# Kernel tuning notes

Measured on AMD Instinct MI355X. Metric: run time of the kernel, lower is better.

Reference implementation:

```python
import jax, jax.numpy as jnp
import numpy as np

S1 = (42, 1600, 1408); S2 = (21, 800, 704); S3 = (11, 400, 352); S4 = (6, 200, 176)
OFF = np.array([[dz, dy, dx] for dz in (-1, 0, 1) for dy in (-1, 0, 1) for dx in (-1, 0, 1)], np.int64)
KOFF = np.array([[kz, ky, kx] for kz in (0, 1, 2) for ky in (0, 1, 2) for kx in (0, 1, 2)], np.int64)

def _keys(c, s):
    return (c[:, 0] * s[1] + c[:, 1]) * s[2] + c[:, 2]

def _lookup(skeys, qk, valid):
    pos = np.searchsorted(skeys, qk)
    posc = np.clip(pos, 0, len(skeys) - 1)
    found = valid & (skeys[posc] == qk)
    return np.where(found, posc, -1).astype(np.int32)

def _subm_nbr(coords, skeys, shape):
    N = len(coords); nbr = np.empty((N, 27), np.int32); sh = np.array(shape)
    for t in range(27):
        q = coords + OFF[t]
        valid = np.all((q >= 0) & (q < sh), axis=1)
        nbr[:, t] = _lookup(skeys, _keys(q, shape), valid)
    return nbr

def _inv_nbr(fcoords, ckeys, cshape):
    # inverse of stride-2, pad-1, k-3 sparse conv: coarse = (fine + 1 - k) / 2
    N = len(fcoords); nbr = np.empty((N, 27), np.int32); csh = np.array(cshape)
    for t in range(27):
        cand = fcoords + 1 - KOFF[t]
        valid = np.all(cand >= 0, axis=1) & np.all(cand % 2 == 0, axis=1)
        cc = cand // 2
        valid &= np.all(cc < csh, axis=1)
        nbr[:, t] = _lookup(ckeys, _keys(cc, cshape), valid)
    return nbr

def _geometry():
    rng = np.random.default_rng(0)
    n = 130000
    c = np.stack([rng.integers(0, S1[i], n) for i in range(3)], 1).astype(np.int64)
    uk, idx = np.unique(_keys(c, S1), return_index=True)
    c1 = c[idx][:100000]; k1 = uk[:len(c1)]
    def down(cf, s):
        cc = cf // 2
        uk, idx = np.unique(_keys(cc, s), return_index=True)
        return cc[idx], uk
    c2, k2 = down(c1, S2); c3, k3 = down(c2, S3); c4, k4 = down(c3, S4)
    return dict(nbr4=_subm_nbr(c4, k4, S4), inv43=_inv_nbr(c3, k4, S4),
                nbr3=_subm_nbr(c3, k3, S3), inv32=_inv_nbr(c2, k3, S3),
                nbr2=_subm_nbr(c2, k2, S2), inv21=_inv_nbr(c1, k2, S2),
                nbr1=_subm_nbr(c1, k1, S1), n4=len(c4), n1=len(c1))

_SPECS = [("m4", 64, 64), ("i4", 64, 64), ("m3", 64, 64), ("i3", 64, 32),
          ("m2", 32, 32), ("i2", 32, 16), ("m1", 16, 16), ("c5", 16, 3)]

def _params(key):
    p = {}
    for i, (nm, ci, co) in enumerate(_SPECS):
        k = jax.random.fold_in(key, i)
        p["W_" + nm] = jax.random.normal(k, (27, ci, co), jnp.float32) * (1.0 / np.sqrt(27.0 * ci))
        p["g_" + nm] = jnp.ones((co,), jnp.float32)
        p["b_" + nm] = jnp.zeros((co,), jnp.float32)
    return p

def setup_inputs() -> dict:
    geo = _geometry()
    key = jax.random.key(0)
    inp = {k: jnp.asarray(v) for k, v in geo.items() if k.startswith(("nbr", "inv"))}
    inp["x"] = jax.random.normal(jax.random.fold_in(key, 100), (geo["n4"], 64), jnp.float32)
    inp.update(_params(key))
    return inp

def _block(f, nbr, W, g, b, relu=True):
    # gather-GEMM (sparse conv), then BatchNorm1d (training mode, eps=1e-3), then ReLU
    m = nbr >= 0                                             # [N,27]
    x = jnp.where(m[..., None], f[jnp.maximum(nbr, 0)], 0.0)  # [N,27,Cin]
    y = jnp.einsum('nkc,kcd->nd', x, W)                      # [N,Cout]
    mu = y.mean(0); var = y.var(0)
    y = (y - mu) * jax.lax.rsqrt(var + 1e-3) * g + b
    return jax.nn.relu(y) if relu else y

def reference(x, nbr4, inv43, nbr3, inv32, nbr2, inv21, nbr1,
              W_m4, g_m4, b_m4, W_i4, g_i4, b_i4, W_m3, g_m3, b_m3, W_i3, g_i3, b_i3,
              W_m2, g_m2, b_m2, W_i2, g_i2, b_i2, W_m1, g_m1, b_m1, W_c5, g_c5, b_c5):
    h = _block(x, nbr4, W_m4, g_m4, b_m4)      # subm4: [N4,64]
    h = _block(h, inv43, W_i4, g_i4, b_i4)     # inverse conv4 -> [N3,64]
    h = _block(h, nbr3, W_m3, g_m3, b_m3)      # subm3
    h = _block(h, inv32, W_i3, g_i3, b_i3)     # inverse conv3 -> [N2,32]
    h = _block(h, nbr2, W_m2, g_m2, b_m2)      # subm2
    h = _block(h, inv21, W_i2, g_i2, b_i2)     # inverse conv2 -> [N1,16]
    h = _block(h, nbr1, W_m1, g_m1, b_m1)      # subm1
    return _block(h, nbr1, W_c5, g_c5, b_c5, relu=False)  # conv5 (shares subm1 rulebook), BN only
```

## Files before the change

### kernel.cpp

```cpp
#include <hip/hip_runtime.h>

typedef _Float16 HALF;
typedef _Float16 f16x8 __attribute__((ext_vector_type(8)));
typedef float f32x4 __attribute__((ext_vector_type(4)));
typedef int i32x4 __attribute__((ext_vector_type(4)));

struct WArgs { const float* W[8]; HALF* dst[8]; };

__global__ void convert_all_w_kernel(WArgs a)
{
    const int CIs[8]  = {64, 64, 64, 64, 32, 32, 16, 16};
    const int COs[8]  = {64, 64, 64, 32, 32, 16, 16, 3};
    const int COPs[8] = {64, 64, 64, 32, 32, 16, 16, 16};
    const int L = blockIdx.y;
    const int CI = CIs[L], CO = COs[L], COP = COPs[L];
    const int K = 27 * CI, KP = (K + 31) & ~31;
    const int total = COP * KP;
    for (int i = blockIdx.x * 256 + threadIdx.x; i < total; i += gridDim.x * 256) {
        int jp = i / KP;
        int kp = i - jp * KP;
        float v = (jp < CO && kp < K) ? a.W[L][(size_t)kp * CO + jp] : 0.f;
        a.dst[L][((size_t)(kp >> 5) * COP + jp) * 32 + (kp & 31)] = (HALF)v;
    }
}

__global__ void convert_x_kernel(const float* __restrict__ x, HALF* __restrict__ xh, int total)
{
    int i = blockIdx.x * 256 + threadIdx.x;
    if (i < total) xh[i] = (HALF)x[i];
}

template<int CI, int CO_PAD, int NMT, bool FUSED>
__global__ __launch_bounds__(256, 2) void conv_kernel(
    const HALF* __restrict__ h, const int* __restrict__ nbr,
    const HALF* __restrict__ Wt, HALF* __restrict__ yout,
    float* __restrict__ sums, int n,
    const float* __restrict__ psums, const float* __restrict__ pg,
    const float* __restrict__ pb, float pinvn)
{
    constexpr int K    = 27 * CI;
    constexpr int KP   = (K + 31) & ~31;
    constexpr int NCH  = KP / 32;
    constexpr int NJB  = CO_PAD / 16;
    constexpr int NW   = 4;
    constexpr int CHK  = (NCH + NW - 1) / NW;
    constexpr int NCB  = (CI >= 64) ? 2 : 1;
    static_assert(NCB == 1 || (CHK & 1) == 0, "parity must stay compile-time");
    constexpr int LOG2CI = (CI == 64) ? 6 : ((CI == 32) ? 5 : 4);
    constexpr int ROWS  = 16 * NMT;
    constexpr int PAIRS = NMT * NJB;
    constexpr int TPW   = CHK / 2;

    __shared__ f32x4 lred[2][PAIRS * 64];
    __shared__ float lscbi[2][64];

    const int wv   = threadIdx.x >> 6;
    const int lane = threadIdx.x & 63;
    const int l15  = lane & 15;
    const int lq   = lane >> 4;

    int bid = blockIdx.x;
    {
        const int nwg = gridDim.x;
        const int q = nwg >> 3, r = nwg & 7;
        const int xcd = bid & 7, idx = bid >> 3;
        bid = (xcd < r ? xcd * (q + 1) : r * (q + 1) + (xcd - r) * q) + idx;
    }
    const int rowBase = bid * ROWS;

    if constexpr (FUSED) {
        const int c = threadIdx.x;
        if (c < CI) {
            float s = 0.f, q = 0.f;
#pragma unroll
            for (int k = 0; k < 8; ++k) { s += psums[k * 128 + c]; q += psums[k * 128 + CI + c]; }
            const float mu  = s * pinvn;
            const float var = q * pinvn - mu * mu;
            const float sc  = rsqrtf(var + 1e-3f) * pg[c];
            lscbi[0][c] = sc;
            lscbi[1][c] = pb[c] - mu * sc;
        }
    }

    f32x4 acc[NMT][NJB];
#pragma unroll
    for (int mt = 0; mt < NMT; ++mt)
#pragma unroll
        for (int jb = 0; jb < NJB; ++jb)
#pragma unroll
            for (int r = 0; r < 4; ++r) acc[mt][jb][r] = 0.f;

    int  nbo[NMT];
    bool rok[NMT];
#pragma unroll
    for (int mt = 0; mt < NMT; ++mt) {
        const int row = rowBase + mt * 16 + l15;
        rok[mt] = row < n;
        nbo[mt] = min(row, n - 1) * 27;
    }

    if constexpr (FUSED) __syncthreads();

    f16x8 sc8[NCB], bi8[NCB];
    if constexpr (FUSED) {
#pragma unroll
        for (int cb = 0; cb < NCB; ++cb) {
            const int c0 = cb * 32 + ((lq * 8) & (CI - 1));
#pragma unroll
            for (int j = 0; j < 8; ++j) {
                sc8[cb][j] = (HALF)lscbi[0][c0 + j];
                bi8[cb][j] = (HALF)lscbi[1][c0 + j];
            }
        }
    }

    if constexpr (CI == 64) {
        const int t0 = wv * TPW;

        int   ipf[2][NMT];
        f16x8 apf[2][NMT][2];
#pragma unroll
        for (int p = 0; p < 2; ++p) {
            const int t = t0 + p;
#pragma unroll
            for (int mt = 0; mt < NMT; ++mt) {
                const int v   = nbr[nbo[mt] + (t < 27 ? t : 26)];
                const int idx = (rok[mt] && t < 27) ? v : -1;
                ipf[p][mt] = idx;
                const HALF* pa = h + ((max(idx, 0) << 6) + lq * 8);
                apf[p][mt][0] = *(const f16x8*)(pa);
                apf[p][mt][1] = *(const f16x8*)(pa + 32);
            }
        }

#pragma unroll
        for (int tt = 0; tt < TPW; ++tt) {
            const int t = t0 + tt;
            if (t >= 27) break;
            const int cur = tt & 1;

            f16x8 a0[NMT], a1[NMT]; int im[NMT];
#pragma unroll
            for (int mt = 0; mt < NMT; ++mt) {
                a0[mt] = apf[cur][mt][0]; a1[mt] = apf[cur][mt][1]; im[mt] = ipf[cur][mt];
            }

            if (tt + 2 < TPW && t + 2 < 27) {
#pragma unroll
                for (int mt = 0; mt < NMT; ++mt) {
                    const int v   = nbr[nbo[mt] + t + 2];
                    const int idx = rok[mt] ? v : -1;
                    ipf[cur][mt] = idx;
                    const HALF* pa = h + ((max(idx, 0) << 6) + lq * 8);
                    apf[cur][mt][0] = *(const f16x8*)(pa);
                    apf[cur][mt][1] = *(const f16x8*)(pa + 32);
                }
            }

            const HALF* wb = Wt + (size_t)(2 * t) * (CO_PAD * 32) + lq * 8;
            f16x8 b0[NJB], b1[NJB];
#pragma unroll
            for (int jb = 0; jb < NJB; ++jb) {
                b0[jb] = *(const f16x8*)(wb + (size_t)(jb * 16 + l15) * 32);
                b1[jb] = *(const f16x8*)(wb + CO_PAD * 32 + (size_t)(jb * 16 + l15) * 32);
            }

#pragma unroll
            for (int mt = 0; mt < NMT; ++mt) {
                f16x8 a = a0[mt];
                if constexpr (FUSED) {
                    a = a * sc8[0] + bi8[0];
#pragma unroll
                    for (int j = 0; j < 8; ++j) a[j] = (a[j] < (HALF)0.f) ? (HALF)0.f : a[j];
                }
                const int m = ~(im[mt] >> 31);
                i32x4 ai = __builtin_bit_cast(i32x4, a);
                ai.x &= m; ai.y &= m; ai.z &= m; ai.w &= m;
                a = __builtin_bit_cast(f16x8, ai);
#pragma unroll
                for (int jb = 0; jb < NJB; ++jb)
                    acc[mt][jb] = __builtin_amdgcn_mfma_f32_16x16x32_f16(a, b0[jb], acc[mt][jb], 0, 0, 0);
            }
#pragma unroll
            for (int mt = 0; mt < NMT; ++mt) {
                f16x8 a = a1[mt];
                if constexpr (FUSED) {
                    a = a * sc8[NCB - 1] + bi8[NCB - 1];
#pragma unroll
                    for (int j = 0; j < 8; ++j) a[j] = (a[j] < (HALF)0.f) ? (HALF)0.f : a[j];
                }
                const int m = ~(im[mt] >> 31);
                i32x4 ai = __builtin_bit_cast(i32x4, a);
                ai.x &= m; ai.y &= m; ai.z &= m; ai.w &= m;
                a = __builtin_bit_cast(f16x8, ai);
#pragma unroll
                for (int jb = 0; jb < NJB; ++jb)
                    acc[mt][jb] = __builtin_amdgcn_mfma_f32_16x16x32_f16(a, b1[jb], acc[mt][jb], 0, 0, 0);
            }
        }
    } else {
        const int kc0 = wv * CHK;

        int   ipf[2][NMT];
        f16x8 apf[2][NMT];
#pragma unroll
        for (int p = 0; p < 2; ++p) {
            const int kc = kc0 + p;
#pragma unroll
            for (int mt = 0; mt < NMT; ++mt) {
                const int t   = (CI == 16) ? (2 * kc + (lq >> 1)) : kc;
                const int v   = nbr[nbo[mt] + (t < 27 ? t : 26)];
                const int idx = (rok[mt] && t < 27) ? v : -1;
                ipf[p][mt] = idx;
                const int c = (CI == 32) ? (lq * 8) : ((lq & 1) * 8);
                apf[p][mt] = *(const f16x8*)(h + ((max(idx, 0) << LOG2CI) + c));
            }
        }

#pragma unroll
        for (int kc2 = 0; kc2 < CHK; ++kc2) {
            const int kc = kc0 + kc2;
            if (kc >= NCH) break;
            const int cur = kc2 & 1;

            const HALF* wb = Wt + (size_t)kc * (CO_PAD * 32) + lq * 8;
            f16x8 b[NJB];
#pragma unroll
            for (int jb = 0; jb < NJB; ++jb)
                b[jb] = *(const f16x8*)(wb + (size_t)(jb * 16 + l15) * 32);

            f16x8 a_use[NMT];
            int   i_use[NMT];
#pragma unroll
            for (int mt = 0; mt < NMT; ++mt) { a_use[mt] = apf[cur][mt]; i_use[mt] = ipf[cur][mt]; }

            if (kc2 + 2 < CHK && kc + 2 < NCH) {
#pragma unroll
                for (int mt = 0; mt < NMT; ++mt) {
                    const int t   = (CI == 16) ? (2 * (kc + 2) + (lq >> 1)) : (kc + 2);
                    const int v   = nbr[nbo[mt] + (t < 27 ? t : 26)];
                    const int idx = (rok[mt] && t < 27) ? v : -1;
                    ipf[cur][mt] = idx;
                    const int c = (CI == 32) ? (lq * 8) : ((lq & 1) * 8);
                    apf[cur][mt] = *(const f16x8*)(h + ((max(idx, 0) << LOG2CI) + c));
                }
            }

#pragma unroll
            for (int mt = 0; mt < NMT; ++mt) {
                f16x8 a = a_use[mt];
                if constexpr (FUSED) {
                    a = a * sc8[0] + bi8[0];
#pragma unroll
                    for (int j = 0; j < 8; ++j) a[j] = (a[j] < (HALF)0.f) ? (HALF)0.f : a[j];
                }
                const int m = ~(i_use[mt] >> 31);
                i32x4 ai = __builtin_bit_cast(i32x4, a);
                ai.x &= m; ai.y &= m; ai.z &= m; ai.w &= m;
                a = __builtin_bit_cast(f16x8, ai);
#pragma unroll
                for (int jb = 0; jb < NJB; ++jb)
                    acc[mt][jb] = __builtin_amdgcn_mfma_f32_16x16x32_f16(a, b[jb], acc[mt][jb], 0, 0, 0);
            }
        }
    }

    if (wv & 1) {
#pragma unroll
        for (int mt = 0; mt < NMT; ++mt)
#pragma unroll
            for (int jb = 0; jb < NJB; ++jb)
                lred[wv >> 1][(mt * NJB + jb) * 64 + lane] = acc[mt][jb];
    }
    __syncthreads();
    if (!(wv & 1)) {
#pragma unroll
        for (int mt = 0; mt < NMT; ++mt)
#pragma unroll
            for (int jb = 0; jb < NJB; ++jb)
                acc[mt][jb] += lred[wv >> 1][(mt * NJB + jb) * 64 + lane];
    }
    __syncthreads();
    if (wv == 2) {
#pragma unroll
        for (int mt = 0; mt < NMT; ++mt)
#pragma unroll
            for (int jb = 0; jb < NJB; ++jb)
                lred[0][(mt * NJB + jb) * 64 + lane] = acc[mt][jb];
    }
    __syncthreads();

    if (wv == 0) {
#pragma unroll
        for (int mt = 0; mt < NMT; ++mt)
#pragma unroll
            for (int jb = 0; jb < NJB; ++jb)
                acc[mt][jb] += lred[0][(mt * NJB + jb) * 64 + lane];

        float* sl = sums + (bid & 7) * 128;
#pragma unroll
        for (int jb = 0; jb < NJB; ++jb) {
            const int col = jb * 16 + l15;
            float s = 0.f, sq = 0.f;
#pragma unroll
            for (int mt = 0; mt < NMT; ++mt) {
                const int rb = rowBase + mt * 16 + lq * 4;
#pragma unroll
                for (int r = 0; r < 4; ++r) {
                    if (rb + r < n) {
                        const float v = acc[mt][jb][r];
                        yout[(size_t)(rb + r) * CO_PAD + col] = (HALF)v;
                        s += v;
                        sq += v * v;
                    }
                }
            }
            s  += __shfl_xor(s, 16);  s  += __shfl_xor(s, 32);
            sq += __shfl_xor(sq, 16); sq += __shfl_xor(sq, 32);
            if (lane < 16) {
                atomicAdd(&sl[col], s);
                atomicAdd(&sl[CO_PAD + col], sq);
            }
        }
    }
}

__global__ void bn_out_kernel(const HALF* __restrict__ y, const float* __restrict__ sums,
                              const float* __restrict__ g, const float* __restrict__ b,
                              int n, float invn, float* __restrict__ out)
{
    int i = blockIdx.x * 256 + threadIdx.x;
    if (i >= n * 3) return;
    int row = i / 3;
    int c = i - row * 3;
    float ssum = 0.f, qsum = 0.f;
#pragma unroll
    for (int k2 = 0; k2 < 8; ++k2) {
        ssum += sums[k2 * 128 + c];
        qsum += sums[k2 * 128 + 16 + c];
    }
    float mu  = ssum * invn;
    float var = qsum * invn - mu * mu;
    float sc  = rsqrtf(var + 1e-3f) * g[c];
    out[i] = ((float)y[(size_t)row * 16 + c] - mu) * sc + b[c];
}

extern "C" void kernel_launch(void* const* d_in, const int* in_sizes, int n_in,
                              void* d_out, int out_size, void* d_ws, size_t ws_size,
                              hipStream_t stream)
{
    const int* nbr4  = (const int*)d_in[0];
    const int* inv43 = (const int*)d_in[1];
    const int* nbr3  = (const int*)d_in[2];
    const int* inv32 = (const int*)d_in[3];
    const int* nbr2  = (const int*)d_in[4];
    const int* inv21 = (const int*)d_in[5];
    const int* nbr1  = (const int*)d_in[6];
    const float* x   = (const float*)d_in[7];

    const int n4 = in_sizes[0] / 27;
    const int n3 = in_sizes[1] / 27;
    const int n2 = in_sizes[3] / 27;
    const int n1 = in_sizes[5] / 27;

    const int CIs[8]  = {64, 64, 64, 64, 32, 32, 16, 16};
    const int COPs[8] = {64, 64, 64, 32, 32, 16, 16, 16};
    int KPs[8], wtoff[8];
    int wtot = 0;
    for (int s = 0; s < 8; ++s) {
        KPs[s] = ((27 * CIs[s] + 31) / 32) * 32;
        wtoff[s] = wtot;
        wtot += COPs[s] * KPs[s];
    }

    char* ws = (char*)d_ws;
    HALF* wt = (HALF*)ws;
    size_t off = ((size_t)wtot * sizeof(HALF) + 255) & ~(size_t)255;
    float* sums = (float*)(ws + off);
    off += 8 * 1024 * sizeof(float);
    off = (off + 255) & ~(size_t)255;
    HALF* xh = (HALF*)(ws + off);
    off += ((size_t)n4 * 64 * sizeof(HALF) + 255) & ~(size_t)255;
    size_t bufElems = 0;
    {
        size_t cand[4] = {(size_t)n4 * 64, (size_t)n3 * 64, (size_t)n2 * 32, (size_t)n1 * 16};
        for (int i = 0; i < 4; ++i) if (cand[i] > bufElems) bufElems = cand[i];
    }
    HALF* Y0 = (HALF*)(ws + off);
    off += (bufElems * sizeof(HALF) + 255) & ~(size_t)255;
    HALF* Y1 = (HALF*)(ws + off);

    hipMemsetAsync(sums, 0, 8 * 1024 * sizeof(float), stream);

    WArgs wa;
    for (int s = 0; s < 8; ++s) { wa.W[s] = (const float*)d_in[8 + 3 * s]; wa.dst[s] = wt + wtoff[s]; }
    {
        int maxTotal = 64 * KPs[0];
        dim3 grid((maxTotal + 255) / 256, 8);
        convert_all_w_kernel<<<grid, 256, 0, stream>>>(wa);
    }
    convert_x_kernel<<<(n4 * 64 + 255) / 256, 256, 0, stream>>>(x, xh, n4 * 64);

#define G(s) ((const float*)d_in[9 + 3 * (s)])
#define B(s) ((const float*)d_in[10 + 3 * (s)])
#define SUMS(s) (sums + (s) * 1024)
#define GRID(nn) (((nn) + 31) / 32)

    conv_kernel<64, 64, 2, false><<<GRID(n4), 256, 0, stream>>>(
        xh, nbr4, wt + wtoff[0], Y0, SUMS(0), n4, nullptr, nullptr, nullptr, 0.f);
    conv_kernel<64, 64, 2, true><<<GRID(n3), 256, 0, stream>>>(
        Y0, inv43, wt + wtoff[1], Y1, SUMS(1), n3, SUMS(0), G(0), B(0), 1.f / n4);
    conv_kernel<64, 64, 2, true><<<GRID(n3), 256, 0, stream>>>(
        Y1, nbr3, wt + wtoff[2], Y0, SUMS(2), n3, SUMS(1), G(1), B(1), 1.f / n3);
    conv_kernel<64, 32, 2, true><<<GRID(n2), 256, 0, stream>>>(
        Y0, inv32, wt + wtoff[3], Y1, SUMS(3), n2, SUMS(2), G(2), B(2), 1.f / n3);
    conv_kernel<32, 32, 2, true><<<GRID(n2), 256, 0, stream>>>(
        Y1, nbr2, wt + wtoff[4], Y0, SUMS(4), n2, SUMS(3), G(3), B(3), 1.f / n2);
    conv_kernel<32, 16, 2, true><<<GRID(n1), 256, 0, stream>>>(
        Y0, inv21, wt + wtoff[5], Y1, SUMS(5), n1, SUMS(4), G(4), B(4), 1.f / n2);
    conv_kernel<16, 16, 2, true><<<GRID(n1), 256, 0, stream>>>(
        Y1, nbr1, wt + wtoff[6], Y0, SUMS(6), n1, SUMS(5), G(5), B(5), 1.f / n1);
    conv_kernel<16, 16, 2, true><<<GRID(n1), 256, 0, stream>>>(
        Y0, nbr1, wt + wtoff[7], Y1, SUMS(7), n1, SUMS(6), G(6), B(6), 1.f / n1);
    bn_out_kernel<<<(n1 * 3 + 255) / 256, 256, 0, stream>>>(
        Y1, SUMS(7), G(7), B(7), n1, 1.f / n1, (float*)d_out);

#undef G
#undef B
#undef SUMS
#undef GRID
}
```

Before: 482.8 us.

## Stage neighbor indices in LDS and skip taps empty across a row tile

Each 32-row block now loads its neighbor indices into shared memory once. It then builds a compacted list of kernel taps that have at least one valid neighbor in the tile, and waves walk only those taps, so gathers, weight loads and MFMAs for fully empty taps are skipped. The geometry is very sparse (random points, inverse convs), so many taps should be empty. In exchange the kernel adds extra barriers, a serial single-thread compaction step, and a dynamic loop that replaces the fully unrolled static prefetch schedule on the non-full paths.

```diff
diff --git a/kernel.cpp b/kernel.cpp
--- a/kernel.cpp
+++ b/kernel.cpp
@@ -30,7 +30,7 @@
     if (i < total) xh[i] = (HALF)x[i];
 }
 
-template<int CI, int CO_PAD, int NMT, bool FUSED>
+template<int CI, int CO_PAD, bool FUSED>
 __global__ __launch_bounds__(256, 2) void conv_kernel(
     const HALF* __restrict__ h, const int* __restrict__ nbr,
     const HALF* __restrict__ Wt, HALF* __restrict__ yout,
@@ -38,21 +38,19 @@
     const float* __restrict__ psums, const float* __restrict__ pg,
     const float* __restrict__ pb, float pinvn)
 {
-    constexpr int K    = 27 * CI;
-    constexpr int KP   = (K + 31) & ~31;
-    constexpr int NCH  = KP / 32;
-    constexpr int NJB  = CO_PAD / 16;
-    constexpr int NW   = 4;
-    constexpr int CHK  = (NCH + NW - 1) / NW;
-    constexpr int NCB  = (CI >= 64) ? 2 : 1;
-    static_assert(NCB == 1 || (CHK & 1) == 0, "parity must stay compile-time");
+    constexpr int NMT   = 2;
+    constexpr int NJB   = CO_PAD / 16;
+    constexpr int NCB   = (CI >= 64) ? 2 : 1;
     constexpr int LOG2CI = (CI == 64) ? 6 : ((CI == 32) ? 5 : 4);
-    constexpr int ROWS  = 16 * NMT;
+    constexpr int ROWS  = 32;
     constexpr int PAIRS = NMT * NJB;
-    constexpr int TPW   = CHK / 2;
 
     __shared__ f32x4 lred[2][PAIRS * 64];
     __shared__ float lscbi[2][64];
+    __shared__ int   lidx[ROWS * 27];
+    __shared__ int   tflag[27];
+    __shared__ int   tls[32];
+    __shared__ int   ntapS;
 
     const int wv   = threadIdx.x >> 6;
     const int lane = threadIdx.x & 63;
@@ -68,6 +66,11 @@
     }
     const int rowBase = bid * ROWS;
 
+    for (int i = threadIdx.x; i < ROWS * 27; i += 256) {
+        const int r   = i / 27;
+        const int row = rowBase + r;
+        lidx[i] = (row < n) ? nbr[(size_t)row * 27 + (i - r * 27)] : -1;
+    }
     if constexpr (FUSED) {
         const int c = threadIdx.x;
         if (c < CI) {
@@ -81,25 +84,23 @@
             lscbi[1][c] = pb[c] - mu * sc;
         }
     }
-
-    f32x4 acc[NMT][NJB];
-#pragma unroll
-    for (int mt = 0; mt < NMT; ++mt)
-#pragma unroll
-        for (int jb = 0; jb < NJB; ++jb)
-#pragma unroll
-            for (int r = 0; r < 4; ++r) acc[mt][jb][r] = 0.f;
-
-    int  nbo[NMT];
-    bool rok[NMT];
-#pragma unroll
-    for (int mt = 0; mt < NMT; ++mt) {
-        const int row = rowBase + mt * 16 + l15;
-        rok[mt] = row < n;
-        nbo[mt] = min(row, n - 1) * 27;
-    }
-
-    if constexpr (FUSED) __syncthreads();
+    __syncthreads();
+
+    if (threadIdx.x < 27) {
+        int any = 0;
+        for (int r = 0; r < ROWS; ++r) any |= ~(lidx[r * 27 + threadIdx.x] >> 31);
+        tflag[threadIdx.x] = any & 1;
+    }
+    __syncthreads();
+    if (threadIdx.x == 0) {
+        int c = 0;
+#pragma unroll
+        for (int t = 0; t < 27; ++t) if (tflag[t]) tls[c++] = t;
+        ntapS = c;
+        for (int t = c; t < 32; ++t) tls[t] = 27;
+    }
+    __syncthreads();
+    const int NT = ntapS;
 
     f16x8 sc8[NCB], bi8[NCB];
     if constexpr (FUSED) {
@@ -114,156 +115,216 @@
         }
     }
 
+    f32x4 acc[NMT][NJB];
+#pragma unroll
+    for (int mt = 0; mt < NMT; ++mt)
+#pragma unroll
+        for (int jb = 0; jb < NJB; ++jb)
+#pragma unroll
+            for (int r = 0; r < 4; ++r) acc[mt][jb][r] = 0.f;
+
+    int lb[NMT];
+#pragma unroll
+    for (int mt = 0; mt < NMT; ++mt) lb[mt] = (mt * 16 + l15) * 27;
+
+    #define CONSUME64(aV_, imV_, bV_, CBIDX_) do { \
+        f16x8 a_ = (aV_); \
+        if constexpr (FUSED) { \
+            a_ = a_ * sc8[CBIDX_] + bi8[CBIDX_]; \
+            _Pragma("unroll") \
+            for (int j_ = 0; j_ < 8; ++j_) a_[j_] = (a_[j_] < (HALF)0.f) ? (HALF)0.f : a_[j_]; \
+        } \
+        const int m_ = ~((imV_) >> 31); \
+        i32x4 ai_ = __builtin_bit_cast(i32x4, a_); \
+        ai_.x &= m_; ai_.y &= m_; ai_.z &= m_; ai_.w &= m_; \
+        a_ = __builtin_bit_cast(f16x8, ai_); \
+        _Pragma("unroll") \
+        for (int jb_ = 0; jb_ < NJB; ++jb_) \
+            acc[mt][jb_] = __builtin_amdgcn_mfma_f32_16x16x32_f16(a_, (bV_)[jb_], acc[mt][jb_], 0, 0, 0); \
+    } while (0)
+
     if constexpr (CI == 64) {
-        const int t0 = wv * TPW;
-
-        int   ipf[2][NMT];
-        f16x8 apf[2][NMT][2];
-#pragma unroll
-        for (int p = 0; p < 2; ++p) {
-            const int t = t0 + p;
+        if (NT == 27) {
+            constexpr int TPW = 7;
+            const int t0 = wv * TPW;
+
+            int   ipf[2][NMT];
+            f16x8 apf[2][NMT][2];
+#pragma unroll
+            for (int p = 0; p < 2; ++p) {
+                const int t = t0 + p;
+#pragma unroll
+                for (int mt = 0; mt < NMT; ++mt) {
+                    const int idx = (t < 27) ? lidx[lb[mt] + (t < 27 ? t : 26)] : -1;
+                    ipf[p][mt] = idx;
+                    const HALF* pa = h + ((max(idx, 0) << 6) + lq * 8);
+                    apf[p][mt][0] = *(const f16x8*)(pa);
+                    apf[p][mt][1] = *(const f16x8*)(pa + 32);
+                }
+            }
+
+#pragma unroll
+            for (int tt = 0; tt < TPW; ++tt) {
+                const int t = t0 + tt;
+                if (t >= 27) break;
+                const int cur = tt & 1;
+
+                f16x8 a0[NMT], a1[NMT]; int im[NMT];
+#pragma unroll
+                for (int mt = 0; mt < NMT; ++mt) {
+                    a0[mt] = apf[cur][mt][0]; a1[mt] = apf[cur][mt][1]; im[mt] = ipf[cur][mt];
+                }
+
+                if (tt + 2 < TPW && t + 2 < 27) {
+#pragma unroll
+                    for (int mt = 0; mt < NMT; ++mt) {
+                        const int idx = lidx[lb[mt] + t + 2];
+                        ipf[cur][mt] = idx;
+                        const HALF* pa = h + ((max(idx, 0) << 6) + lq * 8);
+                        apf[cur][mt][0] = *(const f16x8*)(pa);
+                        apf[cur][mt][1] = *(const f16x8*)(pa + 32);
+                    }
+                }
+
+                const HALF* wb = Wt + (size_t)(2 * t) * (CO_PAD * 32) + lq * 8;
+                f16x8 b0[NJB], b1[NJB];
+#pragma unroll
+                for (int jb = 0; jb < NJB; ++jb) {
+                    b0[jb] = *(const f16x8*)(wb + (size_t)(jb * 16 + l15) * 32);
+                    b1[jb] = *(const f16x8*)(wb + CO_PAD * 32 + (size_t)(jb * 16 + l15) * 32);
+                }
+
+#pragma unroll
+                for (int mt = 0; mt < NMT; ++mt) CONSUME64(a0[mt], im[mt], b0, 0);
+#pragma unroll
+                for (int mt = 0; mt < NMT; ++mt) CONSUME64(a1[mt], im[mt], b1, NCB - 1);
+            }
+        } else {
+            int ti = wv;
+            int   tcur, icur[NMT];
+            f16x8 a0c[NMT], a1c[NMT];
+            {
+                tcur = tls[ti];
+#pragma unroll
+                for (int mt = 0; mt < NMT; ++mt) {
+                    const int idx = (tcur < 27) ? lidx[lb[mt] + min(tcur, 26)] : -1;
+                    icur[mt] = idx;
+                    const HALF* pa = h + ((max(idx, 0) << 6) + lq * 8);
+                    a0c[mt] = *(const f16x8*)(pa);
+                    a1c[mt] = *(const f16x8*)(pa + 32);
+                }
+            }
+            for (; ti < NT; ti += 4) {
+                int   tnx = tls[min(ti + 4, 31)];
+                int   inx[NMT];
+                f16x8 a0n[NMT], a1n[NMT];
+#pragma unroll
+                for (int mt = 0; mt < NMT; ++mt) {
+                    const int idx = (tnx < 27) ? lidx[lb[mt] + min(tnx, 26)] : -1;
+                    inx[mt] = idx;
+                    const HALF* pa = h + ((max(idx, 0) << 6) + lq * 8);
+                    a0n[mt] = *(const f16x8*)(pa);
+                    a1n[mt] = *(const f16x8*)(pa + 32);
+                }
+
+                const HALF* wb = Wt + (size_t)(2 * tcur) * (CO_PAD * 32) + lq * 8;
+                f16x8 b0[NJB], b1[NJB];
+#pragma unroll
+                for (int jb = 0; jb < NJB; ++jb) {
+                    b0[jb] = *(const f16x8*)(wb + (size_t)(jb * 16 + l15) * 32);
+                    b1[jb] = *(const f16x8*)(wb + CO_PAD * 32 + (size_t)(jb * 16 + l15) * 32);
+                }
+
+#pragma unroll
+                for (int mt = 0; mt < NMT; ++mt) CONSUME64(a0c[mt], icur[mt], b0, 0);
+#pragma unroll
+                for (int mt = 0; mt < NMT; ++mt) CONSUME64(a1c[mt], icur[mt], b1, NCB - 1);
+
+                tcur = tnx;
+#pragma unroll
+                for (int mt = 0; mt < NMT; ++mt) {
+                    icur[mt] = inx[mt]; a0c[mt] = a0n[mt]; a1c[mt] = a1n[mt];
+                }
+            }
+        }
+    } else if constexpr (CI == 32) {
+        int ti = wv;
+        int   tcur, icur[NMT];
+        f16x8 ac[NMT];
+        {
+            tcur = tls[ti];
 #pragma unroll
             for (int mt = 0; mt < NMT; ++mt) {
-                const int v   = nbr[nbo[mt] + (t < 27 ? t : 26)];
-                const int idx = (rok[mt] && t < 27) ? v : -1;
-                ipf[p][mt] = idx;
-                const HALF* pa = h + ((max(idx, 0) << 6) + lq * 8);
-                apf[p][mt][0] = *(const f16x8*)(pa);
-                apf[p][mt][1] = *(const f16x8*)(pa + 32);
-            }
-        }
-
-#pragma unroll
-        for (int tt = 0; tt < TPW; ++tt) {
-            const int t = t0 + tt;
-            if (t >= 27) break;
-            const int cur = tt & 1;
-
-            f16x8 a0[NMT], a1[NMT]; int im[NMT];
+                const int idx = (tcur < 27) ? lidx[lb[mt] + min(tcur, 26)] : -1;
+                icur[mt] = idx;
+                ac[mt] = *(const f16x8*)(h + ((max(idx, 0) << 5) + lq * 8));
+            }
+        }
+        for (; ti < NT; ti += 4) {
+            int   tnx = tls[min(ti + 4, 31)];
+            int   inx[NMT];
+            f16x8 an[NMT];
 #pragma unroll
             for (int mt = 0; mt < NMT; ++mt) {
-                a0[mt] = apf[cur][mt][0]; a1[mt] = apf[cur][mt][1]; im[mt] = ipf[cur][mt];
-            }
-
-            if (tt + 2 < TPW && t + 2 < 27) {
-#pragma unroll
-                for (int mt = 0; mt < NMT; ++mt) {
-                    const int v   = nbr[nbo[mt] + t + 2];
-                    const int idx = rok[mt] ? v : -1;
-                    ipf[cur][mt] = idx;
-                    const HALF* pa = h + ((max(idx, 0) << 6) + lq * 8);
-                    apf[cur][mt][0] = *(const f16x8*)(pa);
-                    apf[cur][mt][1] = *(const f16x8*)(pa + 32);
-                }
-            }
-
-            const HALF* wb = Wt + (size_t)(2 * t) * (CO_PAD * 32) + lq * 8;
-            f16x8 b0[NJB], b1[NJB];
-#pragma unroll
-            for (int jb = 0; jb < NJB; ++jb) {
-                b0[jb] = *(const f16x8*)(wb + (size_t)(jb * 16 + l15) * 32);
-                b1[jb] = *(const f16x8*)(wb + CO_PAD * 32 + (size_t)(jb * 16 + l15) * 32);
-            }
-
+                const int idx = (tnx < 27) ? lidx[lb[mt] + min(tnx, 26)] : -1;
+                inx[mt] = idx;
+                an[mt] = *(const f16x8*)(h + ((max(idx, 0) << 5) + lq * 8));
+            }
+
+            const HALF* wb = Wt + (size_t)tcur * (CO_PAD * 32) + lq * 8;
+            f16x8 b[NJB];
+#pragma unroll
+            for (int jb = 0; jb < NJB; ++jb)
+                b[jb] = *(const f16x8*)(wb + (size_t)(jb * 16 + l15) * 32);
+
+#pragma unroll
+            for (int mt = 0; mt < NMT; ++mt) CONSUME64(ac[mt], icur[mt], b, 0);
+
+            tcur = tnx;
+#pragma unroll
+            for (int mt = 0; mt < NMT; ++mt) { icur[mt] = inx[mt]; ac[mt] = an[mt]; }
+        }
+    } else {
+        const int NS = (NT + 1) >> 1;
+        int ti = wv;
+        int   tcur, icur[NMT];
+        f16x8 ac[NMT];
+        {
+            tcur = tls[min(2 * ti + (lq >> 1), 31)];
 #pragma unroll
             for (int mt = 0; mt < NMT; ++mt) {
-                f16x8 a = a0[mt];
-                if constexpr (FUSED) {
-                    a = a * sc8[0] + bi8[0];
-#pragma unroll
-                    for (int j = 0; j < 8; ++j) a[j] = (a[j] < (HALF)0.f) ? (HALF)0.f : a[j];
-                }
-                const int m = ~(im[mt] >> 31);
-                i32x4 ai = __builtin_bit_cast(i32x4, a);
-                ai.x &= m; ai.y &= m; ai.z &= m; ai.w &= m;
-                a = __builtin_bit_cast(f16x8, ai);
-#pragma unroll
-                for (int jb = 0; jb < NJB; ++jb)
-                    acc[mt][jb] = __builtin_amdgcn_mfma_f32_16x16x32_f16(a, b0[jb], acc[mt][jb], 0, 0, 0);
-            }
+                const int idx = (tcur < 27) ? lidx[lb[mt] + min(tcur, 26)] : -1;
+                icur[mt] = idx;
+                ac[mt] = *(const f16x8*)(h + ((max(idx, 0) << 4) + (lq & 1) * 8));
+            }
+        }
+        for (; ti < NS; ti += 4) {
+            int   tnx = tls[min(2 * (ti + 4) + (lq >> 1), 31)];
+            int   inx[NMT];
+            f16x8 an[NMT];
 #pragma unroll
             for (int mt = 0; mt < NMT; ++mt) {
-                f16x8 a = a1[mt];
-                if constexpr (FUSED) {
-                    a = a * sc8[NCB - 1] + bi8[NCB - 1];
-#pragma unroll
-                    for (int j = 0; j < 8; ++j) a[j] = (a[j] < (HALF)0.f) ? (HALF)0.f : a[j];
-                }
-                const int m = ~(im[mt] >> 31);
-                i32x4 ai = __builtin_bit_cast(i32x4, a);
-                ai.x &= m; ai.y &= m; ai.z &= m; ai.w &= m;
-                a = __builtin_bit_cast(f16x8, ai);
-#pragma unroll
-                for (int jb = 0; jb < NJB; ++jb)
-                    acc[mt][jb] = __builtin_amdgcn_mfma_f32_16x16x32_f16(a, b1[jb], acc[mt][jb], 0, 0, 0);
-            }
-        }
-    } else {
-        const int kc0 = wv * CHK;
-
-        int   ipf[2][NMT];
-        f16x8 apf[2][NMT];
-#pragma unroll
-        for (int p = 0; p < 2; ++p) {
-            const int kc = kc0 + p;
-#pragma unroll
-            for (int mt = 0; mt < NMT; ++mt) {
-                const int t   = (CI == 16) ? (2 * kc + (lq >> 1)) : kc;
-                const int v   = nbr[nbo[mt] + (t < 27 ? t : 26)];
-                const int idx = (rok[mt] && t < 27) ? v : -1;
-                ipf[p][mt] = idx;
-                const int c = (CI == 32) ? (lq * 8) : ((lq & 1) * 8);
-                apf[p][mt] = *(const f16x8*)(h + ((max(idx, 0) << LOG2CI) + c));
-            }
-        }
-
-#pragma unroll
-        for (int kc2 = 0; kc2 < CHK; ++kc2) {
-            const int kc = kc0 + kc2;
-            if (kc >= NCH) break;
-            const int cur = kc2 & 1;
-
-            const HALF* wb = Wt + (size_t)kc * (CO_PAD * 32) + lq * 8;
+                const int idx = (tnx < 27) ? lidx[lb[mt] + min(tnx, 26)] : -1;
+                inx[mt] = idx;
+                an[mt] = *(const f16x8*)(h + ((max(idx, 0) << 4) + (lq & 1) * 8));
+            }
+
+            const int tb = min(tcur, 26);
             f16x8 b[NJB];
 #pragma unroll
             for (int jb = 0; jb < NJB; ++jb)
-                b[jb] = *(const f16x8*)(wb + (size_t)(jb * 16 + l15) * 32);
-
-            f16x8 a_use[NMT];
-            int   i_use[NMT];
-#pragma unroll
-            for (int mt = 0; mt < NMT; ++mt) { a_use[mt] = apf[cur][mt]; i_use[mt] = ipf[cur][mt]; }
-
-            if (kc2 + 2 < CHK && kc + 2 < NCH) {
-#pragma unroll
-                for (int mt = 0; mt < NMT; ++mt) {
-                    const int t   = (CI == 16) ? (2 * (kc + 2) + (lq >> 1)) : (kc + 2);
-                    const int v   = nbr[nbo[mt] + (t < 27 ? t : 26)];
-                    const int idx = (rok[mt] && t < 27) ? v : -1;
-                    ipf[cur][mt] = idx;
-                    const int c = (CI == 32) ? (lq * 8) : ((lq & 1) * 8);
-                    apf[cur][mt] = *(const f16x8*)(h + ((max(idx, 0) << LOG2CI) + c));
-                }
-            }
-
-#pragma unroll
-            for (int mt = 0; mt < NMT; ++mt) {
-                f16x8 a = a_use[mt];
-                if constexpr (FUSED) {
-                    a = a * sc8[0] + bi8[0];
-#pragma unroll
-                    for (int j = 0; j < 8; ++j) a[j] = (a[j] < (HALF)0.f) ? (HALF)0.f : a[j];
-                }
-                const int m = ~(i_use[mt] >> 31);
-                i32x4 ai = __builtin_bit_cast(i32x4, a);
-                ai.x &= m; ai.y &= m; ai.z &= m; ai.w &= m;
-                a = __builtin_bit_cast(f16x8, ai);
-#pragma unroll
-                for (int jb = 0; jb < NJB; ++jb)
-                    acc[mt][jb] = __builtin_amdgcn_mfma_f32_16x16x32_f16(a, b[jb], acc[mt][jb], 0, 0, 0);
-            }
-        }
-    }
+                b[jb] = *(const f16x8*)(Wt + (size_t)(tb >> 1) * (CO_PAD * 32)
+                                        + (size_t)(jb * 16 + l15) * 32 + (tb & 1) * 16 + (lq & 1) * 8);
+
+#pragma unroll
+            for (int mt = 0; mt < NMT; ++mt) CONSUME64(ac[mt], icur[mt], b, 0);
+
+            tcur = tnx;
+#pragma unroll
+            for (int mt = 0; mt < NMT; ++mt) { icur[mt] = inx[mt]; ac[mt] = an[mt]; }
+        }
+    }
+    #undef CONSUME64
 
     if (wv & 1) {
 #pragma unroll
@@ -406,21 +467,21 @@
 #define SUMS(s) (sums + (s) * 1024)
 #define GRID(nn) (((nn) + 31) / 32)
 
-    conv_kernel<64, 64, 2, false><<<GRID(n4), 256, 0, stream>>>(
+    conv_kernel<64, 64, false><<<GRID(n4), 256, 0, stream>>>(
         xh, nbr4, wt + wtoff[0], Y0, SUMS(0), n4, nullptr, nullptr, nullptr, 0.f);
-    conv_kernel<64, 64, 2, true><<<GRID(n3), 256, 0, stream>>>(
+    conv_kernel<64, 64, true><<<GRID(n3), 256, 0, stream>>>(
         Y0, inv43, wt + wtoff[1], Y1, SUMS(1), n3, SUMS(0), G(0), B(0), 1.f / n4);
-    conv_kernel<64, 64, 2, true><<<GRID(n3), 256, 0, stream>>>(
+    conv_kernel<64, 64, true><<<GRID(n3), 256, 0, stream>>>(
         Y1, nbr3, wt + wtoff[2], Y0, SUMS(2), n3, SUMS(1), G(1), B(1), 1.f / n3);
-    conv_kernel<64, 32, 2, true><<<GRID(n2), 256, 0, stream>>>(
+    conv_kernel<64, 32, true><<<GRID(n2), 256, 0, stream>>>(
         Y0, inv32, wt + wtoff[3], Y1, SUMS(3), n2, SUMS(2), G(2), B(2), 1.f / n3);
-    conv_kernel<32, 32, 2, true><<<GRID(n2), 256, 0, stream>>>(
+    conv_kernel<32, 32, true><<<GRID(n2), 256, 0, stream>>>(
         Y1, nbr2, wt + wtoff[4], Y0, SUMS(4), n2, SUMS(3), G(3), B(3), 1.f / n2);
-    conv_kernel<32, 16, 2, true><<<GRID(n1), 256, 0, stream>>>(
+    conv_kernel<32, 16, true><<<GRID(n1), 256, 0, stream>>>(
         Y0, inv21, wt + wtoff[5], Y1, SUMS(5), n1, SUMS(4), G(4), B(4), 1.f / n2);
-    conv_kernel<16, 16, 2, true><<<GRID(n1), 256, 0, stream>>>(
+    conv_kernel<16, 16, true><<<GRID(n1), 256, 0, stream>>>(
         Y1, nbr1, wt + wtoff[6], Y0, SUMS(6), n1, SUMS(5), G(5), B(5), 1.f / n1);
-    conv_kernel<16, 16, 2, true><<<GRID(n1), 256, 0, stream>>>(
+    conv_kernel<16, 16, true><<<GRID(n1), 256, 0, stream>>>(
         Y0, nbr1, wt + wtoff[7], Y1, SUMS(7), n1, SUMS(6), G(6), B(6), 1.f / n1);
     bn_out_kernel<<<(n1 * 3 + 255) / 256, 256, 0, stream>>>(
         Y1, SUMS(7), G(7), B(7), n1, 1.f / n1, (float*)d_out);
```

After: 476.5 us. No clear change (-1.3%).
